# Optimization experiments

Hardware: AMD Instinct MI355X
Metric: run time of the kernel (lower is better)

## Reference

```python
import jax, jax.numpy as jnp
import numpy as np

TOPK = 16  # module init arg
EPS = 1e-12  # F.normalize eps


def setup_inputs() -> dict:
    key = jax.random.key(0)
    k1, k2, k3 = jax.random.split(key, 3)
    b, c, h, w = 2, 256, 96, 96
    rc = max(c // 4, 16)  # reduced_channels = 64
    x = jax.random.normal(k1, (b, c, h, w), dtype=jnp.float32)
    # 1x1 convs are channel-mixing matmuls; store weights as [out_ch, in_ch]
    w_reduce = jax.random.normal(k2, (rc, c), dtype=jnp.float32) * 0.05
    w_proj = jax.random.normal(k3, (c, rc), dtype=jnp.float32) * 0.05
    return {"x": x, "w_reduce": w_reduce, "w_proj": w_proj}


def reference(x, w_reduce, w_proj):
    b, c, h, w = x.shape
    n = h * w
    # reduce: 1x1 conv == channel matmul -> [b, rc, N]
    feat = jnp.einsum('rc,bchw->brhw', w_reduce, x).reshape(b, -1, n)
    # F.normalize(dim=1): divide by max(L2-norm over channels, eps)
    nrm = jnp.maximum(jnp.sqrt(jnp.sum(feat * feat, axis=1, keepdims=True)), EPS)
    nf = jnp.transpose(feat / nrm, (0, 2, 1))  # [b, N, rc]
    # cosine similarity matrix [b, N, N]
    sim = jnp.einsum('bnr,bmr->bnm', nf, nf)
    k = min(TOPK, n)
    _, idx = jax.lax.top_k(sim, k)  # [b, N, k]
    # gather top-k neighbor features and average -> [b, N, rc]
    corr = jax.vmap(lambda f, i: f[i].mean(axis=1))(nf, idx)
    # proj: 1x1 conv back to C channels, NCHW layout
    enhanced = jnp.einsum('cr,bnr->bnc', w_proj, corr)
    enhanced = jnp.transpose(enhanced, (0, 2, 1)).reshape(b, c, h, w)
    return x + enhanced
```

## Files before the change

kernel.cpp:

```cpp
#include <hip/hip_runtime.h>
#include <cstdint>
#include <cstddef>

#define NPIX 9216
#define NB 2
#define NC 256
#define RC 64
#define TK 16
#define NROWS (NB * NPIX)
#define CT 128
#define ECOLS 1152
#define NTE 9
#define MAXC 128
#define LCAP 128
#define MARGIN 0.008f

typedef unsigned short ushort_t;
typedef unsigned int uint_t;
typedef __bf16 bf16x8 __attribute__((ext_vector_type(8)));
typedef float f32x4 __attribute__((ext_vector_type(4)));

__device__ __forceinline__ uint_t f2bf(float x) {
  uint_t u = __float_as_uint(x);
  return (u + 0x7FFFu + ((u >> 16) & 1u)) >> 16;
}

__device__ __forceinline__ uint_t ordu(float v) {
  uint_t u = __float_as_uint(v);
  return (u & 0x80000000u) ? ~u : (u | 0x80000000u);
}

__global__ __launch_bounds__(256) void k_reduce(
    const float* __restrict__ x, const float* __restrict__ wr,
    float* __restrict__ feat4) {
  __shared__ float wl[64 * 16];
  const int bi = blockIdx.x;
  const int pg = bi >> 4, rq = (bi >> 2) & 3, cq = bi & 3;
  const int tid = threadIdx.x;
  {
    const int cl = tid >> 2, rg = (tid & 3) * 4;
#pragma unroll
    for (int i = 0; i < 4; ++i)
      wl[cl * 16 + rg + i] = wr[(size_t)(rq * 16 + rg + i) * NC + cq * 64 + cl];
  }
  __syncthreads();

  const int p = pg * 256 + tid;
  const int b = p >= NPIX;
  const int n = p - b * NPIX;
  const float* xp = x + (size_t)b * NC * NPIX + (size_t)cq * 64 * NPIX + n;

  float4 acc[4];
#pragma unroll
  for (int i = 0; i < 4; ++i) acc[i] = make_float4(0.f, 0.f, 0.f, 0.f);

  for (int c = 0; c < 64; ++c) {
    const float xv = xp[(size_t)c * NPIX];
    const float4* w4 = (const float4*)(wl + c * 16);
#pragma unroll
    for (int i = 0; i < 4; ++i) {
      float4 w = w4[i];
      acc[i].x += w.x * xv; acc[i].y += w.y * xv;
      acc[i].z += w.z * xv; acc[i].w += w.w * xv;
    }
  }
  float4* o = (float4*)(feat4 + (((size_t)(rq * 4 + cq)) * NROWS + p) * 16);
#pragma unroll
  for (int i = 0; i < 4; ++i) o[i] = acc[i];
}

__global__ __launch_bounds__(256) void k_normsplit(
    const float* __restrict__ feat4, float* __restrict__ nf,
    ushort_t* __restrict__ hi) {
  const int t = blockIdx.x * 256 + threadIdx.x;
  const int p = t >> 2, q = t & 3;
  float4 v[4];
#pragma unroll
  for (int i = 0; i < 4; ++i) v[i] = make_float4(0.f, 0.f, 0.f, 0.f);
#pragma unroll
  for (int pt = 0; pt < 4; ++pt) {
    const float4* fp = (const float4*)(feat4 + (((size_t)(q * 4 + pt)) * NROWS + p) * 16);
#pragma unroll
    for (int i = 0; i < 4; ++i) {
      float4 a = fp[i];
      v[i].x += a.x; v[i].y += a.y; v[i].z += a.z; v[i].w += a.w;
    }
  }
  float ssq = 0.f;
#pragma unroll
  for (int i = 0; i < 4; ++i)
    ssq += v[i].x * v[i].x + v[i].y * v[i].y + v[i].z * v[i].z + v[i].w * v[i].w;
  ssq += __shfl_xor(ssq, 1);
  ssq += __shfl_xor(ssq, 2);
  const float inv = 1.f / fmaxf(sqrtf(ssq), 1e-12f);

  float s[16];
#pragma unroll
  for (int i = 0; i < 4; ++i) {
    s[i * 4 + 0] = v[i].x * inv; s[i * 4 + 1] = v[i].y * inv;
    s[i * 4 + 2] = v[i].z * inv; s[i * 4 + 3] = v[i].w * inv;
  }
  float4* no = (float4*)(nf + (size_t)p * RC + q * 16);
#pragma unroll
  for (int i = 0; i < 4; ++i)
    no[i] = make_float4(s[i * 4], s[i * 4 + 1], s[i * 4 + 2], s[i * 4 + 3]);

  uint_t hs[16];
#pragma unroll
  for (int i = 0; i < 16; ++i) hs[i] = f2bf(s[i]);
  uint4* ho = (uint4*)(hi + (size_t)p * RC + q * 16);
#pragma unroll
  for (int h = 0; h < 2; ++h)
    ho[h] = make_uint4(hs[h*8+0] | (hs[h*8+1] << 16), hs[h*8+2] | (hs[h*8+3] << 16),
                       hs[h*8+4] | (hs[h*8+5] << 16), hs[h*8+6] | (hs[h*8+7] << 16));
}

__global__ __launch_bounds__(256) void k_sim_max(
    const ushort_t* __restrict__ nf_hi, float* __restrict__ tmax) {
  __shared__ ushort_t sh[CT * 72];
  const int rb = blockIdx.x >> 3, q = blockIdx.x & 7;
  const int tid = threadIdx.x, wave = tid >> 6, lane = tid & 63;
  const int n = lane & 15, quad = lane >> 4;
  const int r0 = rb * 128 + wave * 32 + n, r1 = r0 + 16;
  const int b = rb >= 72;
  const size_t cbase = (size_t)b * NPIX;

  const bf16x8 bh00 = *(const bf16x8*)(nf_hi + (size_t)r0 * 64 + quad * 8);
  const bf16x8 bh01 = *(const bf16x8*)(nf_hi + (size_t)r0 * 64 + 32 + quad * 8);
  const bf16x8 bh10 = *(const bf16x8*)(nf_hi + (size_t)r1 * 64 + quad * 8);
  const bf16x8 bh11 = *(const bf16x8*)(nf_hi + (size_t)r1 * 64 + 32 + quad * 8);

  const int sc = tid >> 1, sseg = (tid & 1) * 32;
  float cm0 = -1e30f, cm1 = -1e30f;

  for (int t = 0; t < NTE; ++t) {
    const int cb = q * ECOLS + t * CT;
    __syncthreads();
    {
      const uint4* g = (const uint4*)(nf_hi + (cbase + cb + sc) * 64 + sseg);
      uint4* d = (uint4*)(sh + sc * 72 + sseg);
#pragma unroll
      for (int i = 0; i < 4; ++i) d[i] = g[i];
    }
    __syncthreads();

#pragma unroll 2
    for (int st = 0; st < 8; ++st) {
      const ushort_t* ap = sh + (st * 16 + n) * 72 + quad * 8;
      bf16x8 ah0 = *(const bf16x8*)ap;
      bf16x8 ah1 = *(const bf16x8*)(ap + 32);
      f32x4 z = {0.f, 0.f, 0.f, 0.f};
      f32x4 a0 = __builtin_amdgcn_mfma_f32_16x16x32_bf16(ah0, bh00, z, 0, 0, 0);
      a0 = __builtin_amdgcn_mfma_f32_16x16x32_bf16(ah1, bh01, a0, 0, 0, 0);
      f32x4 a1 = __builtin_amdgcn_mfma_f32_16x16x32_bf16(ah0, bh10, z, 0, 0, 0);
      a1 = __builtin_amdgcn_mfma_f32_16x16x32_bf16(ah1, bh11, a1, 0, 0, 0);
      cm0 = fmaxf(cm0, fmaxf(fmaxf(a0[0], a0[1]), fmaxf(a0[2], a0[3])));
      cm1 = fmaxf(cm1, fmaxf(fmaxf(a1[0], a1[1]), fmaxf(a1[2], a1[3])));
    }
    if (t % 3 == 2) {
      const int cn = t / 3;
      tmax[(size_t)r0 * 96 + (q * 4 + quad) * 3 + cn] = cm0;
      tmax[(size_t)r1 * 96 + (q * 4 + quad) * 3 + cn] = cm1;
      cm0 = -1e30f; cm1 = -1e30f;
    }
  }
}

__global__ __launch_bounds__(256) void k_thresh(
    const float* __restrict__ tmax, float* __restrict__ Tb) {
  const int wave = threadIdx.x >> 6, lane = threadIdx.x & 63;
  const int row = blockIdx.x * 4 + wave;
  const float* tp = tmax + (size_t)row * 96;
  float v0 = tp[lane];
  float v1 = (lane < 32) ? tp[64 + lane] : -1e30f;
  float m = -1e30f;
#pragma unroll
  for (int k = 0; k < TK; ++k) {
    float c = fmaxf(v0, v1);
#pragma unroll
    for (int d = 1; d < 64; d <<= 1) c = fmaxf(c, __shfl_xor(c, d));
    m = c;
    if (v0 == m) v0 = -1e30f;
    if (v1 == m) v1 = -1e30f;
  }
  if (lane == 0) Tb[row] = m - MARGIN;
}

__global__ __launch_bounds__(256) void k_collect(
    const ushort_t* __restrict__ nf_hi, const float* __restrict__ Tb,
    int* __restrict__ cidx, int* __restrict__ rowcnt) {
  __shared__ ushort_t sh[CT * 72];
  __shared__ ushort_t lst[128][LCAP + 1];
  __shared__ int lcnt[128];
  const int rb = blockIdx.x >> 3, q = blockIdx.x & 7;
  const int tid = threadIdx.x, wave = tid >> 6, lane = tid & 63;
  const int n = lane & 15, quad = lane >> 4;
  const int rl0 = wave * 32 + n, rl1 = rl0 + 16;
  const int r0 = rb * 128 + rl0, r1 = r0 + 16;
  const int b = rb >= 72;
  const size_t cbase = (size_t)b * NPIX;

  if (tid < 128) lcnt[tid] = 0;

  const bf16x8 bh00 = *(const bf16x8*)(nf_hi + (size_t)r0 * 64 + quad * 8);
  const bf16x8 bh01 = *(const bf16x8*)(nf_hi + (size_t)r0 * 64 + 32 + quad * 8);
  const bf16x8 bh10 = *(const bf16x8*)(nf_hi + (size_t)r1 * 64 + quad * 8);
  const bf16x8 bh11 = *(const bf16x8*)(nf_hi + (size_t)r1 * 64 + 32 + quad * 8);

  const float T0 = Tb[r0], T1 = Tb[r1];
  const int sc = tid >> 1, sseg = (tid & 1) * 32;

  for (int t = 0; t < NTE; ++t) {
    const int cb = q * ECOLS + t * CT;
    __syncthreads();
    {
      const uint4* g = (const uint4*)(nf_hi + (cbase + cb + sc) * 64 + sseg);
      uint4* d = (uint4*)(sh + sc * 72 + sseg);
#pragma unroll
      for (int i = 0; i < 4; ++i) d[i] = g[i];
    }
    __syncthreads();

#pragma unroll 2
    for (int st = 0; st < 8; ++st) {
      const ushort_t* ap = sh + (st * 16 + n) * 72 + quad * 8;
      bf16x8 ah0 = *(const bf16x8*)ap;
      bf16x8 ah1 = *(const bf16x8*)(ap + 32);
      f32x4 z = {0.f, 0.f, 0.f, 0.f};
      f32x4 a0 = __builtin_amdgcn_mfma_f32_16x16x32_bf16(ah0, bh00, z, 0, 0, 0);
      a0 = __builtin_amdgcn_mfma_f32_16x16x32_bf16(ah1, bh01, a0, 0, 0, 0);
      f32x4 a1 = __builtin_amdgcn_mfma_f32_16x16x32_bf16(ah0, bh10, z, 0, 0, 0);
      a1 = __builtin_amdgcn_mfma_f32_16x16x32_bf16(ah1, bh11, a1, 0, 0, 0);

      const int c0 = cb + st * 16 + quad * 4;
      const int m0 = (a0[0] >= T0) | ((a0[1] >= T0) << 1) |
                     ((a0[2] >= T0) << 2) | ((a0[3] >= T0) << 3);
      if (m0) {
        int slot = atomicAdd(&lcnt[rl0], __popc(m0));
#pragma unroll
        for (int r = 0; r < 4; ++r)
          if (m0 & (1 << r)) {
            if (slot < LCAP) lst[rl0][slot] = (ushort_t)(c0 + r);
            ++slot;
          }
      }
      const int m1 = (a1[0] >= T1) | ((a1[1] >= T1) << 1) |
                     ((a1[2] >= T1) << 2) | ((a1[3] >= T1) << 3);
      if (m1) {
        int slot = atomicAdd(&lcnt[rl1], __popc(m1));
#pragma unroll
        for (int r = 0; r < 4; ++r)
          if (m1 & (1 << r)) {
            if (slot < LCAP) lst[rl1][slot] = (ushort_t)(c0 + r);
            ++slot;
          }
      }
    }
  }
  __syncthreads();
  if (tid < 128) {
    const int row = rb * 128 + tid;
    const int cnt = min(lcnt[tid], LCAP);
    int base = atomicAdd(rowcnt + row, cnt);
    for (int j = 0; j < cnt; ++j) {
      const int gs = base + j;
      if (gs < MAXC) cidx[(size_t)row * MAXC + gs] = (int)lst[tid][j];
    }
  }
}

__global__ __launch_bounds__(256) void k_merge_gather(
    const float* __restrict__ nf, const int* __restrict__ cidx,
    const int* __restrict__ rowcnt, float* __restrict__ corr) {
  __shared__ ushort_t selc[4][TK];
  const int wave = threadIdx.x >> 6, lane = threadIdx.x & 63;
  const int row = blockIdx.x * 4 + wave;
  const int b = row >= NPIX;
  const int rl = row - b * NPIX;
  const float* nfb = nf + (size_t)b * NPIX * RC;
  const int C = min(rowcnt[row], MAXC);

  if (lane < TK) selc[wave][lane] = (ushort_t)rl;
  __syncthreads();

  float4 rv[16];
  const float4* r4 = (const float4*)(nf + (size_t)row * RC);
#pragma unroll
  for (int i = 0; i < 16; ++i) rv[i] = r4[i];

  const int* cp = cidx + (size_t)row * MAXC;
  unsigned long long k0 = 0, k1 = 0;
  int c0 = rl, c1 = rl;
  {
    c0 = (lane < C) ? cp[lane] : rl;
    const float4* g = (const float4*)(nfb + (size_t)c0 * RC);
    float s = 0.f;
#pragma unroll
    for (int i = 0; i < 16; ++i) {
      float4 a = g[i];
      s += a.x * rv[i].x + a.y * rv[i].y + a.z * rv[i].z + a.w * rv[i].w;
    }
    if (lane < C)
      k0 = ((unsigned long long)ordu(s) << 32) | (uint_t)(~(uint_t)c0);
  }
  if (C > 64) {
    c1 = (64 + lane < C) ? cp[64 + lane] : rl;
    const float4* g = (const float4*)(nfb + (size_t)c1 * RC);
    float s = 0.f;
#pragma unroll
    for (int i = 0; i < 16; ++i) {
      float4 a = g[i];
      s += a.x * rv[i].x + a.y * rv[i].y + a.z * rv[i].z + a.w * rv[i].w;
    }
    if (64 + lane < C)
      k1 = ((unsigned long long)ordu(s) << 32) | (uint_t)(~(uint_t)c1);
  }

  unsigned long long thr = 0;
#pragma unroll
  for (int bit = 63; bit >= 0; --bit) {
    const unsigned long long cand = thr | (1ull << bit);
    const int cnt = __popcll(__ballot(k0 >= cand)) + __popcll(__ballot(k1 >= cand));
    if (cnt >= TK) thr = cand;
  }
  if (thr != 0) {
    const unsigned long long ml = (lane == 0) ? 0ull : (~0ull >> (64 - lane));
    const unsigned long long b0 = __ballot(k0 >= thr);
    const unsigned long long b1 = __ballot(k1 >= thr);
    const int n0 = __popcll(b0);
    if (k0 >= thr) {
      const int r = __popcll(b0 & ml);
      if (r < TK) selc[wave][r] = (ushort_t)c0;
    }
    if (k1 >= thr) {
      const int r = n0 + __popcll(b1 & ml);
      if (r < TK) selc[wave][r] = (ushort_t)c1;
    }
  }
  __syncthreads();

  float acc = 0.f;
#pragma unroll
  for (int t = 0; t < TK; ++t)
    acc += nfb[(size_t)selc[wave][t] * RC + lane];
  corr[(size_t)row * RC + lane] = acc * 0.0625f;
}

__global__ __launch_bounds__(256) void k_proj_add(
    const float* __restrict__ x, const float* __restrict__ wp,
    const float* __restrict__ corr, float* __restrict__ out) {
  const int pg = blockIdx.x >> 3, cq = blockIdx.x & 7;
  const int tid = threadIdx.x;

  __shared__ float wl[32 * RC];
  {
    const float4* src = (const float4*)(wp + (size_t)cq * 32 * RC);
    float4* dst = (float4*)wl;
#pragma unroll
    for (int i = 0; i < 2; ++i) dst[i * 256 + tid] = src[i * 256 + tid];
  }

  const int p = pg * 256 + tid;
  const int b = p >= NPIX;
  const int n = p - b * NPIX;

  float4 cr[16];
  const float4* c4 = (const float4*)(corr + (size_t)p * RC);
#pragma unroll
  for (int i = 0; i < 16; ++i) cr[i] = c4[i];
  __syncthreads();

  const size_t xb = (size_t)b * NC * NPIX + n;
  for (int cl = 0; cl < 32; ++cl) {
    const float4* w4 = (const float4*)(wl + cl * RC);
    float s = 0.f;
#pragma unroll
    for (int i = 0; i < 16; ++i) {
      float4 w = w4[i];
      s += w.x * cr[i].x + w.y * cr[i].y + w.z * cr[i].z + w.w * cr[i].w;
    }
    const int c = cq * 32 + cl;
    const size_t oi = xb + (size_t)c * NPIX;
    out[oi] = x[oi] + s;
  }
}

extern "C" void kernel_launch(void* const* d_in, const int* in_sizes, int n_in,
                              void* d_out, int out_size, void* d_ws, size_t ws_size,
                              hipStream_t stream) {
  const float* x = (const float*)d_in[0];
  const float* wr = (const float*)d_in[1];
  const float* wp = (const float*)d_in[2];
  float* out = (float*)d_out;

  char* ws = (char*)d_ws;
  float* feat4 = (float*)ws;
  float* tmax = (float*)ws;
  float* corr = (float*)ws;
  float* nf = (float*)(ws + 18874368);
  ushort_t* nf_hi = (ushort_t*)(ws + 23592960);
  float* Tb = (float*)(ws + 25952256);
  int* rowcnt = (int*)(ws + 26025984);
  int* cidx = (int*)(ws + 26099712);

  hipLaunchKernelGGL(k_reduce, dim3(1152), dim3(256), 0, stream, x, wr, feat4);
  hipLaunchKernelGGL(k_normsplit, dim3(288), dim3(256), 0, stream, feat4, nf, nf_hi);
  hipLaunchKernelGGL(k_sim_max, dim3(1152), dim3(256), 0, stream, nf_hi, tmax);
  hipLaunchKernelGGL(k_thresh, dim3(NROWS / 4), dim3(256), 0, stream, tmax, Tb);
  hipMemsetAsync(rowcnt, 0, NROWS * sizeof(int), stream);
  hipLaunchKernelGGL(k_collect, dim3(1152), dim3(256), 0, stream,
                     nf_hi, Tb, cidx, rowcnt);
  hipLaunchKernelGGL(k_merge_gather, dim3(NROWS / 4), dim3(256), 0, stream,
                     nf, cidx, rowcnt, corr);
  hipLaunchKernelGGL(k_proj_add, dim3(576), dim3(256), 0, stream, x, wp, corr, out);
}
```

Measured before the change: 279.6 us.

## Stage similarity tiles via direct global-to-LDS loads with XOR swizzle

Replaces the register-staged copy of each 128-column bf16 tile into padded shared memory with global_load_lds direct transfers into an unpadded, XOR-swizzled layout in both k_sim_max and k_collect. The MFMA fragment reads use matching swizzled offsets to avoid bank conflicts, the inner loop is fully unrolled, and the barrier placement is restructured. The per-row candidate list capacity in LDS is also halved, which reduces shared memory and may raise occupancy but risks truncating candidate lists for rows with many near-threshold values.

```diff
diff --git a/kernel.cpp b/kernel.cpp
--- a/kernel.cpp
+++ b/kernel.cpp
@@ -12,7 +12,7 @@
 #define ECOLS 1152
 #define NTE 9
 #define MAXC 128
-#define LCAP 128
+#define LCAP 64
 #define MARGIN 0.008f
 
 typedef unsigned short ushort_t;
@@ -28,6 +28,26 @@
 __device__ __forceinline__ uint_t ordu(float v) {
   uint_t u = __float_as_uint(v);
   return (u & 0x80000000u) ? ~u : (u | 0x80000000u);
+}
+
+#define GL2LDS(gsrc, ldst)                                                   \
+  __builtin_amdgcn_global_load_lds(                                          \
+      (const __attribute__((address_space(1))) uint_t*)(const void*)(gsrc),  \
+      (__attribute__((address_space(3))) uint_t*)(void*)(ldst), 16, 0, 0)
+
+__device__ __forceinline__ void stage_tile(
+    const ushort_t* __restrict__ nf_hi, size_t cbase, int cb,
+    ushort_t* shbuf, int tid) {
+  const int wave = tid >> 6, l = tid & 63;
+  const int lr = l >> 3;
+  const int ls = (l & 7) ^ lr;
+#pragma unroll
+  for (int i = 0; i < 4; ++i) {
+    const int j = wave * 4 + i;
+    const ushort_t* g = nf_hi + (cbase + (size_t)(cb + j * 8 + lr)) * 64 + ls * 8;
+    ushort_t* d = shbuf + j * 512;
+    GL2LDS(g, d);
+  }
 }
 
 __global__ __launch_bounds__(256) void k_reduce(
@@ -117,45 +137,39 @@
 
 __global__ __launch_bounds__(256) void k_sim_max(
     const ushort_t* __restrict__ nf_hi, float* __restrict__ tmax) {
-  __shared__ ushort_t sh[CT * 72];
+  __shared__ ushort_t sh[CT * 64];
   const int rb = blockIdx.x >> 3, q = blockIdx.x & 7;
   const int tid = threadIdx.x, wave = tid >> 6, lane = tid & 63;
   const int n = lane & 15, quad = lane >> 4;
   const int r0 = rb * 128 + wave * 32 + n, r1 = r0 + 16;
   const int b = rb >= 72;
   const size_t cbase = (size_t)b * NPIX;
+  const int x0 = (quad ^ (n & 7)) * 8;
+  const int x1 = ((quad + 4) ^ (n & 7)) * 8;
 
   const bf16x8 bh00 = *(const bf16x8*)(nf_hi + (size_t)r0 * 64 + quad * 8);
   const bf16x8 bh01 = *(const bf16x8*)(nf_hi + (size_t)r0 * 64 + 32 + quad * 8);
   const bf16x8 bh10 = *(const bf16x8*)(nf_hi + (size_t)r1 * 64 + quad * 8);
   const bf16x8 bh11 = *(const bf16x8*)(nf_hi + (size_t)r1 * 64 + 32 + quad * 8);
 
-  const int sc = tid >> 1, sseg = (tid & 1) * 32;
   float cm0 = -1e30f, cm1 = -1e30f;
 
   for (int t = 0; t < NTE; ++t) {
-    const int cb = q * ECOLS + t * CT;
+    stage_tile(nf_hi, cbase, q * ECOLS + t * CT, sh, tid);
     __syncthreads();
-    {
-      const uint4* g = (const uint4*)(nf_hi + (cbase + cb + sc) * 64 + sseg);
-      uint4* d = (uint4*)(sh + sc * 72 + sseg);
-#pragma unroll
-      for (int i = 0; i < 4; ++i) d[i] = g[i];
-    }
-    __syncthreads();
-
-#pragma unroll 2
+
+#pragma unroll
     for (int st = 0; st < 8; ++st) {
-      const ushort_t* ap = sh + (st * 16 + n) * 72 + quad * 8;
-      bf16x8 ah0 = *(const bf16x8*)ap;
-      bf16x8 ah1 = *(const bf16x8*)(ap + 32);
+      const ushort_t* ap = sh + (st * 16 + n) * 64;
+      bf16x8 ah0 = *(const bf16x8*)(ap + x0);
+      bf16x8 ah1 = *(const bf16x8*)(ap + x1);
       f32x4 z = {0.f, 0.f, 0.f, 0.f};
       f32x4 a0 = __builtin_amdgcn_mfma_f32_16x16x32_bf16(ah0, bh00, z, 0, 0, 0);
       a0 = __builtin_amdgcn_mfma_f32_16x16x32_bf16(ah1, bh01, a0, 0, 0, 0);
       f32x4 a1 = __builtin_amdgcn_mfma_f32_16x16x32_bf16(ah0, bh10, z, 0, 0, 0);
       a1 = __builtin_amdgcn_mfma_f32_16x16x32_bf16(ah1, bh11, a1, 0, 0, 0);
-      cm0 = fmaxf(cm0, fmaxf(fmaxf(a0[0], a0[1]), fmaxf(a0[2], a0[3])));
-      cm1 = fmaxf(cm1, fmaxf(fmaxf(a1[0], a1[1]), fmaxf(a1[2], a1[3])));
+      cm0 = fmaxf(fmaxf(a0[0], a0[1]), fmaxf(fmaxf(a0[2], a0[3]), cm0));
+      cm1 = fmaxf(fmaxf(a1[0], a1[1]), fmaxf(fmaxf(a1[2], a1[3]), cm1));
     }
     if (t % 3 == 2) {
       const int cn = t / 3;
@@ -163,6 +177,7 @@
       tmax[(size_t)r1 * 96 + (q * 4 + quad) * 3 + cn] = cm1;
       cm0 = -1e30f; cm1 = -1e30f;
     }
+    __syncthreads();
   }
 }
 
@@ -189,7 +204,7 @@
 __global__ __launch_bounds__(256) void k_collect(
     const ushort_t* __restrict__ nf_hi, const float* __restrict__ Tb,
     int* __restrict__ cidx, int* __restrict__ rowcnt) {
-  __shared__ ushort_t sh[CT * 72];
+  __shared__ ushort_t sh[CT * 64];
   __shared__ ushort_t lst[128][LCAP + 1];
   __shared__ int lcnt[128];
   const int rb = blockIdx.x >> 3, q = blockIdx.x & 7;
@@ -199,6 +214,8 @@
   const int r0 = rb * 128 + rl0, r1 = r0 + 16;
   const int b = rb >= 72;
   const size_t cbase = (size_t)b * NPIX;
+  const int x0 = (quad ^ (n & 7)) * 8;
+  const int x1 = ((quad + 4) ^ (n & 7)) * 8;
 
   if (tid < 128) lcnt[tid] = 0;
 
@@ -208,24 +225,17 @@
   const bf16x8 bh11 = *(const bf16x8*)(nf_hi + (size_t)r1 * 64 + 32 + quad * 8);
 
   const float T0 = Tb[r0], T1 = Tb[r1];
-  const int sc = tid >> 1, sseg = (tid & 1) * 32;
 
   for (int t = 0; t < NTE; ++t) {
     const int cb = q * ECOLS + t * CT;
+    stage_tile(nf_hi, cbase, cb, sh, tid);
     __syncthreads();
-    {
-      const uint4* g = (const uint4*)(nf_hi + (cbase + cb + sc) * 64 + sseg);
-      uint4* d = (uint4*)(sh + sc * 72 + sseg);
-#pragma unroll
-      for (int i = 0; i < 4; ++i) d[i] = g[i];
-    }
-    __syncthreads();
-
-#pragma unroll 2
+
+#pragma unroll
     for (int st = 0; st < 8; ++st) {
-      const ushort_t* ap = sh + (st * 16 + n) * 72 + quad * 8;
-      bf16x8 ah0 = *(const bf16x8*)ap;
-      bf16x8 ah1 = *(const bf16x8*)(ap + 32);
+      const ushort_t* ap = sh + (st * 16 + n) * 64;
+      bf16x8 ah0 = *(const bf16x8*)(ap + x0);
+      bf16x8 ah1 = *(const bf16x8*)(ap + x1);
       f32x4 z = {0.f, 0.f, 0.f, 0.f};
       f32x4 a0 = __builtin_amdgcn_mfma_f32_16x16x32_bf16(ah0, bh00, z, 0, 0, 0);
       a0 = __builtin_amdgcn_mfma_f32_16x16x32_bf16(ah1, bh01, a0, 0, 0, 0);
@@ -256,8 +266,8 @@
           }
       }
     }
-  }
-  __syncthreads();
+    __syncthreads();
+  }
   if (tid < 128) {
     const int row = rb * 128 + tid;
     const int cnt = min(lcnt[tid], LCAP);
```

New measurement: 273.8 us. 2.1% less time.
